# Performance work log

Measured on AMD Instinct MI355X. Metric: run time of the kernel, lower is better.

The kernel has to match this reference:

```python
import jax, jax.numpy as jnp
import numpy as np

# locally-connected layer dims (padding='valid', stride 1)
FH, FW = 3, 3
SR, SC = 1, 1
H, W, FIN, FOUT = 32, 32, 64, 64
OH = (H - FH) // SR + 1  # 30
OW = (W - FW) // SC + 1  # 30


def _patches(X):
    # X: [N, H, W, FIN] -> [N, OH*OW, FH*FW*FIN], flatten order (fh, fw, fin)
    # matches tf.reshape(X[:, i:i+fh, j:j+fw, :], (N, fh*fw*fin))
    ps = [X[:, di:di + OH * SR:SR, dj:dj + OW * SC:SC, :]
          for di in range(FH) for dj in range(FW)]  # each [N, OH, OW, FIN]
    p = jnp.stack(ps, axis=3)  # [N, OH, OW, FH*FW, FIN]
    return p.reshape(p.shape[0], OH * OW, FH * FW * FIN)


def setup_inputs() -> dict:
    key = jax.random.key(0)
    k1, k2 = jax.random.split(key)
    X = jax.random.normal(k1, (128, H, W, FIN), dtype=jnp.float32)
    # init='sqrt_fan_in': uniform(-1/sqrt(h*w*fin), 1/sqrt(h*w*fin))
    scale = 1.0 / np.sqrt(H * W * FIN)
    filters = jax.random.uniform(k2, (OH * OW, FH * FW * FIN, FOUT),
                                 dtype=jnp.float32, minval=-scale, maxval=scale)
    return {"X": X, "filters": filters}


def reference(X, filters):
    # per-location (unshared) batched matmul:
    # patches [N, L, K] x filters [L, K, FOUT] -> [N, L, FOUT]
    p = _patches(X)
    out = jnp.einsum('nlk,lkf->nlf', p, filters)
    return out.reshape(X.shape[0], OH, OW, FOUT)
```

## Files before the change

### kernel.cpp

```cpp
#include <hip/hip_runtime.h>
#include <hip/hip_bf16.h>
#include <stdint.h>


typedef __attribute__((ext_vector_type(4))) float  f32x4;
typedef __attribute__((ext_vector_type(8))) short  short8;

#define BOFF 16384

__device__ __forceinline__ uint32_t swz_addr(uint32_t row, uint32_t inrow) {
    uint32_t chunk = inrow >> 4;
    uint32_t rem   = inrow & 15u;
    return row * 128u + (((chunk ^ row ^ (row >> 3)) & 7u) << 4) + rem;
}

__device__ __forceinline__ uint16_t f2bf_u(float x) {
    __hip_bfloat16 h = __float2bfloat16(x);
    uint16_t r;
    __builtin_memcpy(&r, &h, 2);
    return r;
}
__device__ __forceinline__ short f2bf(float x) { return (short)f2bf_u(x); }
__device__ __forceinline__ uint32_t pack2bf(float lo, float hi) {
    return (uint32_t)f2bf_u(lo) | ((uint32_t)f2bf_u(hi) << 16);
}

__global__ __launch_bounds__(512, 4)
void lc_mfma_kernel(const float* __restrict__ X,
                    const float* __restrict__ Fl,
                    float* __restrict__ Out) {
    __shared__ __align__(16) unsigned char lds[2][24576];

    const int orig = blockIdx.x;
    const int xcd  = orig & 7;
    const int idx  = orig >> 3;
    const int l    = (xcd < 4 ? xcd * 113 : 452 + (xcd - 4) * 112) + idx;

    const int oi = l / 30;
    const int oj = l % 30;
    const int tid  = threadIdx.x;
    const int lane = tid & 63;
    const int wave = tid >> 6;

    f32x4 acc[4];
#pragma unroll
    for (int n = 0; n < 4; ++n)
        acc[n] = f32x4{0.f, 0.f, 0.f, 0.f};

    const int ar = tid >> 2;
    const int aq = tid & 3;
    const int fq = tid & 15;
    const int kp = tid >> 4;

    const float* Fb = Fl + (size_t)l * (576 * 64);

    float4 av[4];
    float4 bv[2];

#define ISSUE_LOADS(S)                                                          \
    do {                                                                        \
        const int di_ = (S) / 3, dj_ = (S) % 3;                                 \
        const int h_ = oi + di_, w_ = oj + dj_;                                 \
        const float* a_ = X + (((size_t)ar * 32 + h_) * 32 + w_) * 64 + aq*16;  \
        av[0] = ((const float4*)a_)[0]; av[1] = ((const float4*)a_)[1];         \
        av[2] = ((const float4*)a_)[2]; av[3] = ((const float4*)a_)[3];         \
        const float* b_ = Fb + (size_t)(S) * 4096 + (size_t)(kp*2) * 64 + fq*4; \
        bv[0] = *(const float4*)(b_);                                           \
        bv[1] = *(const float4*)(b_ + 64);                                      \
    } while (0)

#define WRITE_LDS(BUF)                                                          \
    do {                                                                        \
        unsigned char* L_ = lds[BUF];                                           \
        short8 p0, p1;                                                          \
        p0[0]=f2bf(av[0].x); p0[1]=f2bf(av[0].y); p0[2]=f2bf(av[0].z); p0[3]=f2bf(av[0].w); \
        p0[4]=f2bf(av[1].x); p0[5]=f2bf(av[1].y); p0[6]=f2bf(av[1].z); p0[7]=f2bf(av[1].w); \
        p1[0]=f2bf(av[2].x); p1[1]=f2bf(av[2].y); p1[2]=f2bf(av[2].z); p1[3]=f2bf(av[2].w); \
        p1[4]=f2bf(av[3].x); p1[5]=f2bf(av[3].y); p1[6]=f2bf(av[3].z); p1[7]=f2bf(av[3].w); \
        *(short8*)&L_[swz_addr(ar, aq*32 + 0 )] = p0;                           \
        *(short8*)&L_[swz_addr(ar, aq*32 + 16)] = p1;                           \
         \
        *(uint32_t*)&L_[BOFF + swz_addr(fq*4 + 0, kp*4)] = pack2bf(bv[0].x, bv[1].x); \
        *(uint32_t*)&L_[BOFF + swz_addr(fq*4 + 1, kp*4)] = pack2bf(bv[0].y, bv[1].y); \
        *(uint32_t*)&L_[BOFF + swz_addr(fq*4 + 2, kp*4)] = pack2bf(bv[0].z, bv[1].z); \
        *(uint32_t*)&L_[BOFF + swz_addr(fq*4 + 3, kp*4)] = pack2bf(bv[0].w, bv[1].w); \
    } while (0)

    ISSUE_LOADS(0);
    WRITE_LDS(0);

    const int mb   = wave * 16;
    const int rsel = lane & 15;
    const int ksel = (lane >> 4) * 16;

#pragma unroll 1
    for (int s = 0; s < 9; ++s) {
        if (s < 8) ISSUE_LOADS(s + 1);

        __syncthreads();

        const unsigned char* L = lds[s & 1];
#pragma unroll
        for (int kk = 0; kk < 2; ++kk) {
            const uint32_t inrow = (uint32_t)(kk * 64 + ksel);
            const short8 a0 = *(const short8*)&L[swz_addr(mb + rsel, inrow)];
            const short8 b0 = *(const short8*)&L[BOFF + swz_addr(     rsel, inrow)];
            const short8 b1 = *(const short8*)&L[BOFF + swz_addr(16 + rsel, inrow)];
            const short8 b2 = *(const short8*)&L[BOFF + swz_addr(32 + rsel, inrow)];
            const short8 b3 = *(const short8*)&L[BOFF + swz_addr(48 + rsel, inrow)];
            acc[0] = __builtin_amdgcn_mfma_f32_16x16x32_bf16(a0, b0, acc[0], 0, 0, 0);
            acc[1] = __builtin_amdgcn_mfma_f32_16x16x32_bf16(a0, b1, acc[1], 0, 0, 0);
            acc[2] = __builtin_amdgcn_mfma_f32_16x16x32_bf16(a0, b2, acc[2], 0, 0, 0);
            acc[3] = __builtin_amdgcn_mfma_f32_16x16x32_bf16(a0, b3, acc[3], 0, 0, 0);
        }

        if (s < 8) WRITE_LDS((s + 1) & 1);
    }

    const int col = lane & 15;
    const int rb  = (lane >> 4) * 4;
#pragma unroll
    for (int n = 0; n < 4; ++n)
#pragma unroll
        for (int i = 0; i < 4; ++i) {
            const int row = mb + rb + i;
            const int f   = n * 16 + col;
            Out[((size_t)row * 900 + l) * 64 + f] = acc[n][i];
        }
}

extern "C" void kernel_launch(void* const* d_in, const int* in_sizes, int n_in,
                              void* d_out, int out_size, void* d_ws, size_t ws_size,
                              hipStream_t stream) {
    const float* X  = (const float*)d_in[0];
    const float* Fl = (const float*)d_in[1];
    float* Out = (float*)d_out;
    lc_mfma_kernel<<<dim3(900), dim3(512), 0, stream>>>(X, Fl, Out);
}
```

Measured before the change: 40.45 us.

## Stream X tiles directly to LDS via global_load_lds with deeper B prefetch

The activation patch tile is now copied as fp32 straight from global memory into swizzled LDS using global_load_lds, and converted to bf16 only when read for the MFMA. This removes the register staging and conversion on the store side. The filter loads are prefetched two stages ahead using alternating register buffers, and the synchronisation uses explicit vmcnt waits. The trade-off is a larger LDS footprint (80 KB, with the occupancy hint dropped), which limits blocks per CU, plus repeated per-wave conversion work at read time.

```diff
diff --git a/kernel.cpp b/kernel.cpp
--- a/kernel.cpp
+++ b/kernel.cpp
@@ -6,7 +6,12 @@
 typedef __attribute__((ext_vector_type(4))) float  f32x4;
 typedef __attribute__((ext_vector_type(8))) short  short8;
 
-#define BOFF 16384
+typedef __attribute__((address_space(1))) void as1_void;
+typedef __attribute__((address_space(3))) void as3_void;
+
+__device__ __forceinline__ void gload16(const void* g, void* l) {
+    __builtin_amdgcn_global_load_lds((as1_void*)g, (as3_void*)l, 16, 0, 0);
+}
 
 __device__ __forceinline__ uint32_t swz_addr(uint32_t row, uint32_t inrow) {
     uint32_t chunk = inrow >> 4;
@@ -25,11 +30,11 @@
     return (uint32_t)f2bf_u(lo) | ((uint32_t)f2bf_u(hi) << 16);
 }
 
-__global__ __launch_bounds__(512, 4)
+__global__ __launch_bounds__(512)
 void lc_mfma_kernel(const float* __restrict__ X,
                     const float* __restrict__ Fl,
                     float* __restrict__ Out) {
-    __shared__ __align__(16) unsigned char lds[2][24576];
+    __shared__ __align__(16) unsigned char lds[81920];
 
     const int orig = blockIdx.x;
     const int xcd  = orig & 7;
@@ -47,74 +52,100 @@
     for (int n = 0; n < 4; ++n)
         acc[n] = f32x4{0.f, 0.f, 0.f, 0.f};
 
-    const int ar = tid >> 2;
-    const int aq = tid & 3;
+    const int lrow = lane >> 4;
+    const int lchk = lane & 15;
+
     const int fq = tid & 15;
     const int kp = tid >> 4;
-
     const float* Fb = Fl + (size_t)l * (576 * 64);
 
-    float4 av[4];
-    float4 bv[2];
+    const char* Xb = (const char*)X;
 
-#define ISSUE_LOADS(S)                                                          \
+    const int rsel = lane & 15;
+    const int kg   = lane >> 4;
+    const int mb   = wave * 16;
+    const int ksel = kg * 16;
+
+    float4 bvA[2], bvB[2];
+
+#define ISSUE_A(S, BUF)                                                         \
     do {                                                                        \
-        const int di_ = (S) / 3, dj_ = (S) % 3;                                 \
-        const int h_ = oi + di_, w_ = oj + dj_;                                 \
-        const float* a_ = X + (((size_t)ar * 32 + h_) * 32 + w_) * 64 + aq*16;  \
-        av[0] = ((const float4*)a_)[0]; av[1] = ((const float4*)a_)[1];         \
-        av[2] = ((const float4*)a_)[2]; av[3] = ((const float4*)a_)[3];         \
-        const float* b_ = Fb + (size_t)(S) * 4096 + (size_t)(kp*2) * 64 + fq*4; \
-        bv[0] = *(const float4*)(b_);                                           \
-        bv[1] = *(const float4*)(b_ + 64);                                      \
+        const int h_ = oi + (S) / 3, w_ = oj + (S) % 3;                         \
+        const size_t pix_ = ((size_t)(h_ * 32 + w_)) * 256;                     \
+        unsigned char* ab_ = &lds[(BUF) * 32768u];                              \
+        _Pragma("unroll")                                                       \
+        for (int i_ = 0; i_ < 4; ++i_) {                                        \
+            const int row_ = wave * 16 + i_ * 4 + lrow;                         \
+            const uint32_t sc_ = (uint32_t)(lchk ^ (row_ & 15));                \
+            gload16(Xb + (size_t)row_ * 262144 + pix_ + (sc_ << 4),             \
+                    ab_ + (wave * 16 + i_ * 4) * 256);                          \
+        }                                                                       \
     } while (0)
 
-#define WRITE_LDS(BUF)                                                          \
+#define ISSUE_B(S, BV)                                                          \
     do {                                                                        \
-        unsigned char* L_ = lds[BUF];                                           \
-        short8 p0, p1;                                                          \
-        p0[0]=f2bf(av[0].x); p0[1]=f2bf(av[0].y); p0[2]=f2bf(av[0].z); p0[3]=f2bf(av[0].w); \
-        p0[4]=f2bf(av[1].x); p0[5]=f2bf(av[1].y); p0[6]=f2bf(av[1].z); p0[7]=f2bf(av[1].w); \
-        p1[0]=f2bf(av[2].x); p1[1]=f2bf(av[2].y); p1[2]=f2bf(av[2].z); p1[3]=f2bf(av[2].w); \
-        p1[4]=f2bf(av[3].x); p1[5]=f2bf(av[3].y); p1[6]=f2bf(av[3].z); p1[7]=f2bf(av[3].w); \
-        *(short8*)&L_[swz_addr(ar, aq*32 + 0 )] = p0;                           \
-        *(short8*)&L_[swz_addr(ar, aq*32 + 16)] = p1;                           \
-         \
-        *(uint32_t*)&L_[BOFF + swz_addr(fq*4 + 0, kp*4)] = pack2bf(bv[0].x, bv[1].x); \
-        *(uint32_t*)&L_[BOFF + swz_addr(fq*4 + 1, kp*4)] = pack2bf(bv[0].y, bv[1].y); \
-        *(uint32_t*)&L_[BOFF + swz_addr(fq*4 + 2, kp*4)] = pack2bf(bv[0].z, bv[1].z); \
-        *(uint32_t*)&L_[BOFF + swz_addr(fq*4 + 3, kp*4)] = pack2bf(bv[0].w, bv[1].w); \
+        const float* b_ = Fb + (size_t)((S) * 64 + 2 * kp) * 64 + fq * 4;       \
+        BV[0] = *(const float4*)(b_);                                           \
+        BV[1] = *(const float4*)(b_ + 64);                                      \
     } while (0)
 
-    ISSUE_LOADS(0);
-    WRITE_LDS(0);
+#define WRITE_B(S, BV)                                                          \
+    do {                                                                        \
+        unsigned char* L_ = &lds[65536u + ((S) & 1) * 8192u];                   \
+        *(uint32_t*)&L_[swz_addr(fq*4 + 0, kp*4)] = pack2bf(BV[0].x, BV[1].x);  \
+        *(uint32_t*)&L_[swz_addr(fq*4 + 1, kp*4)] = pack2bf(BV[0].y, BV[1].y);  \
+        *(uint32_t*)&L_[swz_addr(fq*4 + 2, kp*4)] = pack2bf(BV[0].z, BV[1].z);  \
+        *(uint32_t*)&L_[swz_addr(fq*4 + 3, kp*4)] = pack2bf(BV[0].w, BV[1].w);  \
+    } while (0)
 
-    const int mb   = wave * 16;
-    const int rsel = lane & 15;
-    const int ksel = (lane >> 4) * 16;
+    ISSUE_B(0, bvA);
+    ISSUE_A(0, 0);
+    ISSUE_B(1, bvB);
+    WRITE_B(0, bvA);
 
 #pragma unroll 1
     for (int s = 0; s < 9; ++s) {
-        if (s < 8) ISSUE_LOADS(s + 1);
+        if (s < 8) asm volatile("s_waitcnt vmcnt(2) lgkmcnt(0)" ::: "memory");
+        else       asm volatile("s_waitcnt vmcnt(0) lgkmcnt(0)" ::: "memory");
+        __builtin_amdgcn_sched_barrier(0);
+        __builtin_amdgcn_s_barrier();
+        __builtin_amdgcn_sched_barrier(0);
 
-        __syncthreads();
-
-        const unsigned char* L = lds[s & 1];
-#pragma unroll
-        for (int kk = 0; kk < 2; ++kk) {
-            const uint32_t inrow = (uint32_t)(kk * 64 + ksel);
-            const short8 a0 = *(const short8*)&L[swz_addr(mb + rsel, inrow)];
-            const short8 b0 = *(const short8*)&L[BOFF + swz_addr(     rsel, inrow)];
-            const short8 b1 = *(const short8*)&L[BOFF + swz_addr(16 + rsel, inrow)];
-            const short8 b2 = *(const short8*)&L[BOFF + swz_addr(32 + rsel, inrow)];
-            const short8 b3 = *(const short8*)&L[BOFF + swz_addr(48 + rsel, inrow)];
-            acc[0] = __builtin_amdgcn_mfma_f32_16x16x32_bf16(a0, b0, acc[0], 0, 0, 0);
-            acc[1] = __builtin_amdgcn_mfma_f32_16x16x32_bf16(a0, b1, acc[1], 0, 0, 0);
-            acc[2] = __builtin_amdgcn_mfma_f32_16x16x32_bf16(a0, b2, acc[2], 0, 0, 0);
-            acc[3] = __builtin_amdgcn_mfma_f32_16x16x32_bf16(a0, b3, acc[3], 0, 0, 0);
+        if (s < 8) ISSUE_A(s + 1, (s + 1) & 1);
+        if (s < 7) {
+            if ((s & 1) == 0) ISSUE_B(s + 2, bvA);
+            else              ISSUE_B(s + 2, bvB);
         }
 
-        if (s < 8) WRITE_LDS((s + 1) & 1);
+        {
+            const unsigned char* LA = &lds[(s & 1) * 32768u];
+            const unsigned char* LB = &lds[65536u + (s & 1) * 8192u];
+#pragma unroll
+            for (int kk = 0; kk < 2; ++kk) {
+                const int cf = kk * 8 + kg * 2;
+                const int ar = mb + rsel;
+                const int rx = ar & 15;
+                const f32x4 fa0 = *(const f32x4*)&LA[(uint32_t)(ar * 256 + ((cf ^ rx) << 4))];
+                const f32x4 fa1 = *(const f32x4*)&LA[(uint32_t)(ar * 256 + (((cf + 1) ^ rx) << 4))];
+                short8 af;
+                af[0]=f2bf(fa0[0]); af[1]=f2bf(fa0[1]); af[2]=f2bf(fa0[2]); af[3]=f2bf(fa0[3]);
+                af[4]=f2bf(fa1[0]); af[5]=f2bf(fa1[1]); af[6]=f2bf(fa1[2]); af[7]=f2bf(fa1[3]);
+                const uint32_t inrow = (uint32_t)(kk * 64 + ksel);
+                const short8 b0 = *(const short8*)&LB[swz_addr(     rsel, inrow)];
+                const short8 b1 = *(const short8*)&LB[swz_addr(16 + rsel, inrow)];
+                const short8 b2 = *(const short8*)&LB[swz_addr(32 + rsel, inrow)];
+                const short8 b3 = *(const short8*)&LB[swz_addr(48 + rsel, inrow)];
+                acc[0] = __builtin_amdgcn_mfma_f32_16x16x32_bf16(af, b0, acc[0], 0, 0, 0);
+                acc[1] = __builtin_amdgcn_mfma_f32_16x16x32_bf16(af, b1, acc[1], 0, 0, 0);
+                acc[2] = __builtin_amdgcn_mfma_f32_16x16x32_bf16(af, b2, acc[2], 0, 0, 0);
+                acc[3] = __builtin_amdgcn_mfma_f32_16x16x32_bf16(af, b3, acc[3], 0, 0, 0);
+            }
+        }
+
+        if (s < 8) {
+            if (((s + 1) & 1) == 0) WRITE_B(s + 1, bvA);
+            else                    WRITE_B(s + 1, bvB);
+        }
     }
 
     const int col = lane & 15;
```

Measured after the change: 43.57 us. +7.7%, slower.
